# Kernel optimization log

Hardware: AMD Instinct MI355X
Metric: run time of the kernel (lower is better)

## Reference

```python
import jax, jax.numpy as jnp
import numpy as np

IN_FEATURES = 4096
OUT_FEATURES = 11008
BATCH = 2048


def setup_inputs() -> dict:
    key = jax.random.key(0)
    k1, k2, k3, k4 = jax.random.split(key, 4)
    # int8-range activations, stored as int32 for exact integer accumulation
    input = jax.random.randint(k1, (BATCH, IN_FEATURES), -127, 128, dtype=jnp.int32)
    # ternary weights in {-1, 0, 1}
    ternary_weight = jax.random.randint(k2, (OUT_FEATURES, IN_FEATURES), -1, 2, dtype=jnp.int32)
    weight_scale = jax.random.uniform(k3, (OUT_FEATURES, 1), dtype=jnp.float32, minval=0.01, maxval=0.1)
    bias = jax.random.normal(k4, (OUT_FEATURES,), dtype=jnp.float32) * 0.01
    return {"input": input, "ternary_weight": ternary_weight,
            "weight_scale": weight_scale, "bias": bias}


def reference(input, ternary_weight, weight_scale, bias):
    # Equivalent to the per-column add/sub loop: int32 accumulate of
    # input @ ternary_weight.T, since w in {-1,0,1}.
    acc = jnp.einsum('bi,oi->bo', input, ternary_weight)  # int32 [B, O]
    out = acc.astype(jnp.float32) * weight_scale.reshape(1, -1)
    out = out + bias
    return out
```

## Files before the change

kernel.cpp:

```cpp
#include <hip/hip_runtime.h>
#include <stdint.h>

#define BATCH   2048
#define KDIM    4096
#define NDIM    11008

#define BM 128
#define BN 128
#define BK 128
#define NT (KDIM / BK)
#define BPK_ROWB 1024

#define A0_OFF 0
#define A1_OFF 16384
#define B_BASE 32768

typedef __attribute__((ext_vector_type(4))) int i32x4;

typedef const __attribute__((address_space(1))) char glob_char;
typedef __attribute__((address_space(3))) char lds_char;

__device__ __forceinline__ unsigned pack4(i32x4 v) {
  return  ((unsigned)v.x & 0xFFu)
        | (((unsigned)v.y & 0xFFu) << 8)
        | (((unsigned)v.z & 0xFFu) << 16)
        | (((unsigned)v.w)         << 24);
}

__global__ __launch_bounds__(256) void convert_i32_i8(const int* __restrict__ src,
                                                      unsigned* __restrict__ dst,
                                                      int n4) {
  int idx = blockIdx.x * 256 + threadIdx.x;
  if (idx >= n4) return;
  i32x4 v = ((const i32x4*)src)[idx];
  dst[idx] = pack4(v);
}

__global__ __launch_bounds__(256) void convert_w2(const int* __restrict__ src,
                                                  unsigned* __restrict__ dst) {
  const int f = blockIdx.x * 256 + threadIdx.x;
  const int r = f >> 8;
  const int i = f & 255;
  const int* p = src + (size_t)r * KDIM + i * 16;
  unsigned w = 0;
#pragma unroll
  for (int e = 0; e < 16; ++e) {
    const unsigned v = (unsigned)p[e] & 3u;
    w |= v << (8 * (e & 3) + 2 * (e >> 2));
  }
  const int slot = (i & 7) ^ (r & 7);
  dst[(size_t)r * 256 + (i >> 3) * 8 + slot] = w;
}

__device__ __forceinline__ i32x4 dec2(unsigned w) {
  const unsigned M1 = 0x01010101u, M2 = 0x02020202u;
  i32x4 r;
  { unsigned x = w;      unsigned y = x & M2; r.x = (int)((x & M1) | ((y << 7) - y)); }
  { unsigned x = w >> 2; unsigned y = x & M2; r.y = (int)((x & M1) | ((y << 7) - y)); }
  { unsigned x = w >> 4; unsigned y = x & M2; r.z = (int)((x & M1) | ((y << 7) - y)); }
  { unsigned x = w >> 6; unsigned y = x & M2; r.w = (int)((x & M1) | ((y << 7) - y)); }
  return r;
}

__global__ __launch_bounds__(256, 3) void ternary_gemm(const char* __restrict__ A8,
                                                       const unsigned* __restrict__ B2,
                                                       const float* __restrict__ scale,
                                                       const float* __restrict__ bias,
                                                       float* __restrict__ out) {
  __shared__ char lds[49152];

  const int tid  = threadIdx.x;
  const int wid  = tid >> 6;
  const int lane = tid & 63;

  const int wg  = (blockIdx.x & 7) * 172 + (blockIdx.x >> 3);
  const int mtq = wg / 344;
  const int r   = wg - mtq * 344;
  const int nt  = r >> 2;
  const int mt  = mtq * 4 + (r & 3);
  const int arow0 = mt * BM;
  const int brow0 = nt * BN;

  const int wc = wid;
  const int rsub = lane & 15;
  const int sgrp = lane >> 4;

  const int srowA = tid >> 3;
  const int slotA = (tid & 7) ^ (srowA & 7);
  const int srowB = tid >> 1;
  const int shalfB = (tid & 1) * 16;

  const char* gAbase = A8 + (size_t)(arow0 + srowA) * KDIM + slotA * 16;
  const char* gBbase = (const char*)B2 + (size_t)(brow0 + srowB) * BPK_ROWB + shalfB;

  auto stageA = [&](int Adst, int kt) {
#pragma unroll
    for (int rr = 0; rr < 4; ++rr) {
      __builtin_amdgcn_global_load_lds(
          (glob_char*)(gAbase + (size_t)rr * 32 * KDIM + kt * BK),
          (lds_char*)(lds + Adst + rr * 4096 + wid * 1024), 16, 0, 0);
    }
  };
  auto stageB = [&](int Bdst, int kt) {
    __builtin_amdgcn_global_load_lds(
        (glob_char*)(gBbase + kt * (BK / 4)),
        (lds_char*)(lds + Bdst + wid * 1024), 16, 0, 0);
  };

  int offA[8][2], offB[2][2];
#pragma unroll
  for (int m = 0; m < 8; ++m) {
    const int row = m * 16 + rsub;
#pragma unroll
    for (int ks = 0; ks < 2; ++ks) {
      const int p = (ks * 4 + sgrp) ^ (row & 7);
      offA[m][ks] = row * 128 + p * 16;
    }
  }
#pragma unroll
  for (int n = 0; n < 2; ++n) {
    const int row = wc * 32 + n * 16 + rsub;
#pragma unroll
    for (int ks = 0; ks < 2; ++ks) {
      const int p = (ks * 4 + sgrp) ^ (row & 7);
      offB[n][ks] = row * 32 + p * 4;
    }
  }

  i32x4 acc[8][2];
#pragma unroll
  for (int m = 0; m < 8; ++m)
#pragma unroll
    for (int n = 0; n < 2; ++n)
      acc[m][n] = (i32x4){0, 0, 0, 0};

  stageA(A0_OFF, 0);
  stageB(B_BASE, 0);
  stageB(B_BASE + 4096, 1);
  asm volatile("s_waitcnt vmcnt(0)" ::: "memory");
  __builtin_amdgcn_s_barrier();

  auto step = [&](int Acur, int Anxt, int Bcur, int Bpf, int t) {
    const int ktA = (t + 1 < NT) ? t + 1 : NT - 1;
    const int ktB = (t + 2 < NT) ? t + 2 : NT - 1;
    stageA(Anxt, ktA);
    stageB(Bpf, ktB);
#pragma unroll
    for (int ks = 0; ks < 2; ++ks) {
      i32x4 a0 = *(const i32x4*)(lds + Acur + offA[0][ks]);
      i32x4 a1 = *(const i32x4*)(lds + Acur + offA[1][ks]);
      i32x4 a2 = *(const i32x4*)(lds + Acur + offA[2][ks]);
      i32x4 a3 = *(const i32x4*)(lds + Acur + offA[3][ks]);
      i32x4 a4 = *(const i32x4*)(lds + Acur + offA[4][ks]);
      i32x4 a5 = *(const i32x4*)(lds + Acur + offA[5][ks]);
      i32x4 a6 = *(const i32x4*)(lds + Acur + offA[6][ks]);
      i32x4 a7 = *(const i32x4*)(lds + Acur + offA[7][ks]);
      unsigned w0 = *(const unsigned*)(lds + Bcur + offB[0][ks]);
      unsigned w1 = *(const unsigned*)(lds + Bcur + offB[1][ks]);
      i32x4 b0 = dec2(w0);
      i32x4 b1 = dec2(w1);
      __builtin_amdgcn_s_setprio(1);
      acc[0][0] = __builtin_amdgcn_mfma_i32_16x16x64_i8(a0, b0, acc[0][0], 0, 0, 0);
      acc[1][0] = __builtin_amdgcn_mfma_i32_16x16x64_i8(a1, b0, acc[1][0], 0, 0, 0);
      acc[2][0] = __builtin_amdgcn_mfma_i32_16x16x64_i8(a2, b0, acc[2][0], 0, 0, 0);
      acc[3][0] = __builtin_amdgcn_mfma_i32_16x16x64_i8(a3, b0, acc[3][0], 0, 0, 0);
      acc[4][0] = __builtin_amdgcn_mfma_i32_16x16x64_i8(a4, b0, acc[4][0], 0, 0, 0);
      acc[5][0] = __builtin_amdgcn_mfma_i32_16x16x64_i8(a5, b0, acc[5][0], 0, 0, 0);
      acc[6][0] = __builtin_amdgcn_mfma_i32_16x16x64_i8(a6, b0, acc[6][0], 0, 0, 0);
      acc[7][0] = __builtin_amdgcn_mfma_i32_16x16x64_i8(a7, b0, acc[7][0], 0, 0, 0);
      acc[0][1] = __builtin_amdgcn_mfma_i32_16x16x64_i8(a0, b1, acc[0][1], 0, 0, 0);
      acc[1][1] = __builtin_amdgcn_mfma_i32_16x16x64_i8(a1, b1, acc[1][1], 0, 0, 0);
      acc[2][1] = __builtin_amdgcn_mfma_i32_16x16x64_i8(a2, b1, acc[2][1], 0, 0, 0);
      acc[3][1] = __builtin_amdgcn_mfma_i32_16x16x64_i8(a3, b1, acc[3][1], 0, 0, 0);
      acc[4][1] = __builtin_amdgcn_mfma_i32_16x16x64_i8(a4, b1, acc[4][1], 0, 0, 0);
      acc[5][1] = __builtin_amdgcn_mfma_i32_16x16x64_i8(a5, b1, acc[5][1], 0, 0, 0);
      acc[6][1] = __builtin_amdgcn_mfma_i32_16x16x64_i8(a6, b1, acc[6][1], 0, 0, 0);
      acc[7][1] = __builtin_amdgcn_mfma_i32_16x16x64_i8(a7, b1, acc[7][1], 0, 0, 0);
      __builtin_amdgcn_s_setprio(0);
    }
    asm volatile("s_waitcnt vmcnt(1)" ::: "memory");
    __builtin_amdgcn_s_barrier();
  };

  for (int t4 = 0; t4 < NT; t4 += 4) {
    step(A0_OFF, A1_OFF, B_BASE,         B_BASE +  8192, t4);
    step(A1_OFF, A0_OFF, B_BASE +  4096, B_BASE + 12288, t4 + 1);
    step(A0_OFF, A1_OFF, B_BASE +  8192, B_BASE,         t4 + 2);
    step(A1_OFF, A0_OFF, B_BASE + 12288, B_BASE +  4096, t4 + 3);
  }

  const int crow = sgrp * 4;
#pragma unroll
  for (int n = 0; n < 2; ++n) {
    const int col = brow0 + wc * 32 + n * 16 + rsub;
    const float sc = scale[col];
    const float bs = bias[col];
#pragma unroll
    for (int m = 0; m < 8; ++m) {
      const int r0 = arow0 + m * 16 + crow;
#pragma unroll
      for (int j = 0; j < 4; ++j) {
        out[(size_t)(r0 + j) * NDIM + col] = (float)acc[m][n][j] * sc + bs;
      }
    }
  }
}

extern "C" void kernel_launch(void* const* d_in, const int* in_sizes, int n_in,
                              void* d_out, int out_size, void* d_ws, size_t ws_size,
                              hipStream_t stream) {
  const int*   input  = (const int*)d_in[0];
  const int*   weight = (const int*)d_in[1];
  const float* scale  = (const float*)d_in[2];
  const float* bias   = (const float*)d_in[3];
  float*       out    = (float*)d_out;

  const size_t needA = (size_t)BATCH * KDIM;

  char*     A8  = (char*)d_ws;
  unsigned* Bpk = (unsigned*)(A8 + needA);
  const int nA4 = (int)(needA / 4);
  convert_i32_i8<<<(nA4 + 255) / 256, 256, 0, stream>>>(input, (unsigned*)A8, nA4);
  convert_w2<<<NDIM * (KDIM / 16) / 256, 256, 0, stream>>>(weight, Bpk);

  const dim3 grid((BATCH / BM) * (NDIM / BN));
  const dim3 block(256);
  ternary_gemm<<<grid, block, 0, stream>>>(A8, Bpk, scale, bias, out);
  (void)ws_size; (void)n_in; (void)in_sizes; (void)out_size;
}
```

Baseline: 138.2 us.

## Load packed ternary weights straight into registers, bypassing LDS staging

The packing kernel now writes the 2-bit weights in a tile-major layout, one contiguous 4 KB block per 128-row by 128-K tile. The GEMM kernel loads each wave's weight fragments directly from global memory into registers, double-buffered two K-tiles ahead. This removes the B-operand LDS staging, its LDS reads and its buffer rotation, and shrinks shared memory. The cost is small 4-byte global loads per lane whose latency must be hidden by the register prefetch. It also relies on the compiler's waitcnt handling for those registers, which could add stalls.

```diff
diff --git a/kernel.cpp b/kernel.cpp
--- a/kernel.cpp
+++ b/kernel.cpp
@@ -9,11 +9,9 @@
 #define BN 128
 #define BK 128
 #define NT (KDIM / BK)
-#define BPK_ROWB 1024
 
 #define A0_OFF 0
 #define A1_OFF 16384
-#define B_BASE 32768
 
 typedef __attribute__((ext_vector_type(4))) int i32x4;
 
@@ -48,8 +46,11 @@
     const unsigned v = (unsigned)p[e] & 3u;
     w |= v << (8 * (e & 3) + 2 * (e >> 2));
   }
-  const int slot = (i & 7) ^ (r & 7);
-  dst[(size_t)r * 256 + (i >> 3) * 8 + slot] = w;
+  const int ntq   = r >> 7;
+  const int rowin = r & 127;
+  const int kt    = i >> 3;
+  const int j     = i & 7;
+  dst[(size_t)ntq * 32768 + kt * 1024 + rowin * 8 + j] = w;
 }
 
 __device__ __forceinline__ i32x4 dec2(unsigned w) {
@@ -63,11 +64,11 @@
 }
 
 __global__ __launch_bounds__(256, 3) void ternary_gemm(const char* __restrict__ A8,
-                                                       const unsigned* __restrict__ B2,
+                                                       const unsigned* __restrict__ B3,
                                                        const float* __restrict__ scale,
                                                        const float* __restrict__ bias,
                                                        float* __restrict__ out) {
-  __shared__ char lds[49152];
+  __shared__ char lds[41088];
 
   const int tid  = threadIdx.x;
   const int wid  = tid >> 6;
@@ -87,11 +88,7 @@
 
   const int srowA = tid >> 3;
   const int slotA = (tid & 7) ^ (srowA & 7);
-  const int srowB = tid >> 1;
-  const int shalfB = (tid & 1) * 16;
-
   const char* gAbase = A8 + (size_t)(arow0 + srowA) * KDIM + slotA * 16;
-  const char* gBbase = (const char*)B2 + (size_t)(brow0 + srowB) * BPK_ROWB + shalfB;
 
   auto stageA = [&](int Adst, int kt) {
 #pragma unroll
@@ -101,13 +98,11 @@
           (lds_char*)(lds + Adst + rr * 4096 + wid * 1024), 16, 0, 0);
     }
   };
-  auto stageB = [&](int Bdst, int kt) {
-    __builtin_amdgcn_global_load_lds(
-        (glob_char*)(gBbase + kt * (BK / 4)),
-        (lds_char*)(lds + Bdst + wid * 1024), 16, 0, 0);
-  };
-
-  int offA[8][2], offB[2][2];
+
+  const char* gB = (const char*)B3 + (size_t)nt * 131072
+                 + (wc * 32 + rsub) * 32 + sgrp * 4;
+
+  int offA[8][2];
 #pragma unroll
   for (int m = 0; m < 8; ++m) {
     const int row = m * 16 + rsub;
@@ -117,15 +112,6 @@
       offA[m][ks] = row * 128 + p * 16;
     }
   }
-#pragma unroll
-  for (int n = 0; n < 2; ++n) {
-    const int row = wc * 32 + n * 16 + rsub;
-#pragma unroll
-    for (int ks = 0; ks < 2; ++ks) {
-      const int p = (ks * 4 + sgrp) ^ (row & 7);
-      offB[n][ks] = row * 32 + p * 4;
-    }
-  }
 
   i32x4 acc[8][2];
 #pragma unroll
@@ -134,59 +120,101 @@
     for (int n = 0; n < 2; ++n)
       acc[m][n] = (i32x4){0, 0, 0, 0};
 
+  unsigned u0, u1, u2, u3, v0, v1, v2, v3;
+
   stageA(A0_OFF, 0);
-  stageB(B_BASE, 0);
-  stageB(B_BASE + 4096, 1);
-  asm volatile("s_waitcnt vmcnt(0)" ::: "memory");
+  u0 = *(const unsigned*)(gB);
+  u1 = *(const unsigned*)(gB + 512);
+  u2 = *(const unsigned*)(gB + 16);
+  u3 = *(const unsigned*)(gB + 528);
+  v0 = *(const unsigned*)(gB + 4096);
+  v1 = *(const unsigned*)(gB + 4096 + 512);
+  v2 = *(const unsigned*)(gB + 4096 + 16);
+  v3 = *(const unsigned*)(gB + 4096 + 528);
+  asm volatile("s_waitcnt vmcnt(4)" ::: "memory");
   __builtin_amdgcn_s_barrier();
 
-  auto step = [&](int Acur, int Anxt, int Bcur, int Bpf, int t) {
+  auto step = [&](int Acur, int Anxt,
+                  unsigned& c0, unsigned& c1, unsigned& c2, unsigned& c3, int t) {
     const int ktA = (t + 1 < NT) ? t + 1 : NT - 1;
     const int ktB = (t + 2 < NT) ? t + 2 : NT - 1;
     stageA(Anxt, ktA);
-    stageB(Bpf, ktB);
-#pragma unroll
-    for (int ks = 0; ks < 2; ++ks) {
-      i32x4 a0 = *(const i32x4*)(lds + Acur + offA[0][ks]);
-      i32x4 a1 = *(const i32x4*)(lds + Acur + offA[1][ks]);
-      i32x4 a2 = *(const i32x4*)(lds + Acur + offA[2][ks]);
-      i32x4 a3 = *(const i32x4*)(lds + Acur + offA[3][ks]);
-      i32x4 a4 = *(const i32x4*)(lds + Acur + offA[4][ks]);
-      i32x4 a5 = *(const i32x4*)(lds + Acur + offA[5][ks]);
-      i32x4 a6 = *(const i32x4*)(lds + Acur + offA[6][ks]);
-      i32x4 a7 = *(const i32x4*)(lds + Acur + offA[7][ks]);
-      unsigned w0 = *(const unsigned*)(lds + Bcur + offB[0][ks]);
-      unsigned w1 = *(const unsigned*)(lds + Bcur + offB[1][ks]);
-      i32x4 b0 = dec2(w0);
-      i32x4 b1 = dec2(w1);
+
+    i32x4 b00 = dec2(c0);
+    i32x4 b10 = dec2(c1);
+    i32x4 b01 = dec2(c2);
+    i32x4 b11 = dec2(c3);
+
+    const char* gBt = gB + (size_t)ktB * 4096;
+    c0 = *(const unsigned*)(gBt);
+    c1 = *(const unsigned*)(gBt + 512);
+    c2 = *(const unsigned*)(gBt + 16);
+    c3 = *(const unsigned*)(gBt + 528);
+
+    {
+      i32x4 a0 = *(const i32x4*)(lds + Acur + offA[0][0]);
+      i32x4 a1 = *(const i32x4*)(lds + Acur + offA[1][0]);
+      i32x4 a2 = *(const i32x4*)(lds + Acur + offA[2][0]);
+      i32x4 a3 = *(const i32x4*)(lds + Acur + offA[3][0]);
+      i32x4 a4 = *(const i32x4*)(lds + Acur + offA[4][0]);
+      i32x4 a5 = *(const i32x4*)(lds + Acur + offA[5][0]);
+      i32x4 a6 = *(const i32x4*)(lds + Acur + offA[6][0]);
+      i32x4 a7 = *(const i32x4*)(lds + Acur + offA[7][0]);
       __builtin_amdgcn_s_setprio(1);
-      acc[0][0] = __builtin_amdgcn_mfma_i32_16x16x64_i8(a0, b0, acc[0][0], 0, 0, 0);
-      acc[1][0] = __builtin_amdgcn_mfma_i32_16x16x64_i8(a1, b0, acc[1][0], 0, 0, 0);
-      acc[2][0] = __builtin_amdgcn_mfma_i32_16x16x64_i8(a2, b0, acc[2][0], 0, 0, 0);
-      acc[3][0] = __builtin_amdgcn_mfma_i32_16x16x64_i8(a3, b0, acc[3][0], 0, 0, 0);
-      acc[4][0] = __builtin_amdgcn_mfma_i32_16x16x64_i8(a4, b0, acc[4][0], 0, 0, 0);
-      acc[5][0] = __builtin_amdgcn_mfma_i32_16x16x64_i8(a5, b0, acc[5][0], 0, 0, 0);
-      acc[6][0] = __builtin_amdgcn_mfma_i32_16x16x64_i8(a6, b0, acc[6][0], 0, 0, 0);
-      acc[7][0] = __builtin_amdgcn_mfma_i32_16x16x64_i8(a7, b0, acc[7][0], 0, 0, 0);
-      acc[0][1] = __builtin_amdgcn_mfma_i32_16x16x64_i8(a0, b1, acc[0][1], 0, 0, 0);
-      acc[1][1] = __builtin_amdgcn_mfma_i32_16x16x64_i8(a1, b1, acc[1][1], 0, 0, 0);
-      acc[2][1] = __builtin_amdgcn_mfma_i32_16x16x64_i8(a2, b1, acc[2][1], 0, 0, 0);
-      acc[3][1] = __builtin_amdgcn_mfma_i32_16x16x64_i8(a3, b1, acc[3][1], 0, 0, 0);
-      acc[4][1] = __builtin_amdgcn_mfma_i32_16x16x64_i8(a4, b1, acc[4][1], 0, 0, 0);
-      acc[5][1] = __builtin_amdgcn_mfma_i32_16x16x64_i8(a5, b1, acc[5][1], 0, 0, 0);
-      acc[6][1] = __builtin_amdgcn_mfma_i32_16x16x64_i8(a6, b1, acc[6][1], 0, 0, 0);
-      acc[7][1] = __builtin_amdgcn_mfma_i32_16x16x64_i8(a7, b1, acc[7][1], 0, 0, 0);
+      acc[0][0] = __builtin_amdgcn_mfma_i32_16x16x64_i8(a0, b00, acc[0][0], 0, 0, 0);
+      acc[1][0] = __builtin_amdgcn_mfma_i32_16x16x64_i8(a1, b00, acc[1][0], 0, 0, 0);
+      acc[2][0] = __builtin_amdgcn_mfma_i32_16x16x64_i8(a2, b00, acc[2][0], 0, 0, 0);
+      acc[3][0] = __builtin_amdgcn_mfma_i32_16x16x64_i8(a3, b00, acc[3][0], 0, 0, 0);
+      acc[4][0] = __builtin_amdgcn_mfma_i32_16x16x64_i8(a4, b00, acc[4][0], 0, 0, 0);
+      acc[5][0] = __builtin_amdgcn_mfma_i32_16x16x64_i8(a5, b00, acc[5][0], 0, 0, 0);
+      acc[6][0] = __builtin_amdgcn_mfma_i32_16x16x64_i8(a6, b00, acc[6][0], 0, 0, 0);
+      acc[7][0] = __builtin_amdgcn_mfma_i32_16x16x64_i8(a7, b00, acc[7][0], 0, 0, 0);
+      acc[0][1] = __builtin_amdgcn_mfma_i32_16x16x64_i8(a0, b10, acc[0][1], 0, 0, 0);
+      acc[1][1] = __builtin_amdgcn_mfma_i32_16x16x64_i8(a1, b10, acc[1][1], 0, 0, 0);
+      acc[2][1] = __builtin_amdgcn_mfma_i32_16x16x64_i8(a2, b10, acc[2][1], 0, 0, 0);
+      acc[3][1] = __builtin_amdgcn_mfma_i32_16x16x64_i8(a3, b10, acc[3][1], 0, 0, 0);
+      acc[4][1] = __builtin_amdgcn_mfma_i32_16x16x64_i8(a4, b10, acc[4][1], 0, 0, 0);
+      acc[5][1] = __builtin_amdgcn_mfma_i32_16x16x64_i8(a5, b10, acc[5][1], 0, 0, 0);
+      acc[6][1] = __builtin_amdgcn_mfma_i32_16x16x64_i8(a6, b10, acc[6][1], 0, 0, 0);
+      acc[7][1] = __builtin_amdgcn_mfma_i32_16x16x64_i8(a7, b10, acc[7][1], 0, 0, 0);
       __builtin_amdgcn_s_setprio(0);
     }
-    asm volatile("s_waitcnt vmcnt(1)" ::: "memory");
+    {
+      i32x4 a0 = *(const i32x4*)(lds + Acur + offA[0][1]);
+      i32x4 a1 = *(const i32x4*)(lds + Acur + offA[1][1]);
+      i32x4 a2 = *(const i32x4*)(lds + Acur + offA[2][1]);
+      i32x4 a3 = *(const i32x4*)(lds + Acur + offA[3][1]);
+      i32x4 a4 = *(const i32x4*)(lds + Acur + offA[4][1]);
+      i32x4 a5 = *(const i32x4*)(lds + Acur + offA[5][1]);
+      i32x4 a6 = *(const i32x4*)(lds + Acur + offA[6][1]);
+      i32x4 a7 = *(const i32x4*)(lds + Acur + offA[7][1]);
+      __builtin_amdgcn_s_setprio(1);
+      acc[0][0] = __builtin_amdgcn_mfma_i32_16x16x64_i8(a0, b01, acc[0][0], 0, 0, 0);
+      acc[1][0] = __builtin_amdgcn_mfma_i32_16x16x64_i8(a1, b01, acc[1][0], 0, 0, 0);
+      acc[2][0] = __builtin_amdgcn_mfma_i32_16x16x64_i8(a2, b01, acc[2][0], 0, 0, 0);
+      acc[3][0] = __builtin_amdgcn_mfma_i32_16x16x64_i8(a3, b01, acc[3][0], 0, 0, 0);
+      acc[4][0] = __builtin_amdgcn_mfma_i32_16x16x64_i8(a4, b01, acc[4][0], 0, 0, 0);
+      acc[5][0] = __builtin_amdgcn_mfma_i32_16x16x64_i8(a5, b01, acc[5][0], 0, 0, 0);
+      acc[6][0] = __builtin_amdgcn_mfma_i32_16x16x64_i8(a6, b01, acc[6][0], 0, 0, 0);
+      acc[7][0] = __builtin_amdgcn_mfma_i32_16x16x64_i8(a7, b01, acc[7][0], 0, 0, 0);
+      acc[0][1] = __builtin_amdgcn_mfma_i32_16x16x64_i8(a0, b11, acc[0][1], 0, 0, 0);
+      acc[1][1] = __builtin_amdgcn_mfma_i32_16x16x64_i8(a1, b11, acc[1][1], 0, 0, 0);
+      acc[2][1] = __builtin_amdgcn_mfma_i32_16x16x64_i8(a2, b11, acc[2][1], 0, 0, 0);
+      acc[3][1] = __builtin_amdgcn_mfma_i32_16x16x64_i8(a3, b11, acc[3][1], 0, 0, 0);
+      acc[4][1] = __builtin_amdgcn_mfma_i32_16x16x64_i8(a4, b11, acc[4][1], 0, 0, 0);
+      acc[5][1] = __builtin_amdgcn_mfma_i32_16x16x64_i8(a5, b11, acc[5][1], 0, 0, 0);
+      acc[6][1] = __builtin_amdgcn_mfma_i32_16x16x64_i8(a6, b11, acc[6][1], 0, 0, 0);
+      acc[7][1] = __builtin_amdgcn_mfma_i32_16x16x64_i8(a7, b11, acc[7][1], 0, 0, 0);
+      __builtin_amdgcn_s_setprio(0);
+    }
+
+    asm volatile("s_waitcnt vmcnt(4)" ::: "memory");
     __builtin_amdgcn_s_barrier();
   };
 
-  for (int t4 = 0; t4 < NT; t4 += 4) {
-    step(A0_OFF, A1_OFF, B_BASE,         B_BASE +  8192, t4);
-    step(A1_OFF, A0_OFF, B_BASE +  4096, B_BASE + 12288, t4 + 1);
-    step(A0_OFF, A1_OFF, B_BASE +  8192, B_BASE,         t4 + 2);
-    step(A1_OFF, A0_OFF, B_BASE + 12288, B_BASE +  4096, t4 + 3);
+  for (int t2 = 0; t2 < NT; t2 += 2) {
+    step(A0_OFF, A1_OFF, u0, u1, u2, u3, t2);
+    step(A1_OFF, A0_OFF, v0, v1, v2, v3, t2 + 1);
   }
 
   const int crow = sgrp * 4;
```

Result: slower. 173.9 us (+25.8%).
